# Optimization experiments

Hardware: AMD Instinct MI355X
Metric: run time of the kernel (lower is better)

## Reference

```python
import jax, jax.numpy as jnp
import numpy as np

D_MODEL = 768
NUM_HEADS = 12
D_K = D_MODEL // NUM_HEADS
B, S = 8, 1024


def setup_inputs() -> dict:
    key = jax.random.key(0)
    ks = jax.random.split(key, 10)
    sc = 1.0 / np.sqrt(D_MODEL)
    inp = {
        'x': jax.random.normal(ks[0], (B, S, D_MODEL), dtype=jnp.float32),
        'mask': jnp.tril(jnp.ones((1, 1, S, S), dtype=jnp.int32)),
        'W_q': jax.random.normal(ks[1], (D_MODEL, D_MODEL), jnp.float32) * sc,
        'b_q': jnp.zeros((D_MODEL,), jnp.float32),
        'W_k': jax.random.normal(ks[2], (D_MODEL, D_MODEL), jnp.float32) * sc,
        'b_k': jnp.zeros((D_MODEL,), jnp.float32),
        'W_v': jax.random.normal(ks[3], (D_MODEL, D_MODEL), jnp.float32) * sc,
        'b_v': jnp.zeros((D_MODEL,), jnp.float32),
        'W_o': jax.random.normal(ks[4], (D_MODEL, D_MODEL), jnp.float32) * sc,
        'b_o': jnp.zeros((D_MODEL,), jnp.float32),
    }
    return inp


def reference(x, mask, W_q, b_q, W_k, b_k, W_v, b_v, W_o, b_o):
    b, s, d = x.shape
    # project (torch Linear: y = x @ W.T + b; here weights stored as [in, out])
    q = (x @ W_q + b_q).reshape(b, s, NUM_HEADS, D_K).transpose(0, 2, 1, 3)
    k = (x @ W_k + b_k).reshape(b, s, NUM_HEADS, D_K).transpose(0, 2, 1, 3)
    v = (x @ W_v + b_v).reshape(b, s, NUM_HEADS, D_K).transpose(0, 2, 1, 3)
    scores = jnp.einsum('bhqd,bhkd->bhqk', q, k) / jnp.sqrt(jnp.float32(D_K))
    scores = jnp.where(mask == 0, jnp.float32(-jnp.inf), scores)
    attn = jax.nn.softmax(scores, axis=-1)  # dropout: eval mode (identity)
    out = jnp.einsum('bhqk,bhkd->bhqd', attn, v)
    out = out.transpose(0, 2, 1, 3).reshape(b, s, d)
    return out @ W_o + b_o
```

## Files before the change

### kernel.cpp

```cpp
#include <hip/hip_runtime.h>
#include <hip/hip_bf16.h>
#include <stdint.h>

typedef __attribute__((ext_vector_type(8))) short short8;
typedef __attribute__((ext_vector_type(4))) short s16x4;
typedef __attribute__((ext_vector_type(4))) float f32x4;

#define GLDS16(gp, lp) __builtin_amdgcn_global_load_lds( \
    (const __attribute__((address_space(1))) void*)(gp), \
    (__attribute__((address_space(3))) void*)(lp), 16, 0, 0)

__device__ __forceinline__ unsigned short f2bf(float f) {
  union { float f; unsigned u; } v; v.f = f;
  unsigned r = v.u + 0x7FFFu + ((v.u >> 16) & 1u);
  return (unsigned short)(r >> 16);
}

__device__ __forceinline__ short bfpack(float f) {
  union { float f; unsigned u; } v; v.f = f;
  return (short)((v.u + 0x8000u) >> 16);
}

__global__ __launch_bounds__(256) void cast_x(const float* __restrict__ x,
                                              unsigned short* __restrict__ o, int n4) {
  int i = blockIdx.x * 256 + threadIdx.x;
  if (i < n4) {
    float4 v = ((const float4*)x)[i];
    union { unsigned short u[4]; unsigned long long ll; } r;
    r.u[0] = f2bf(v.x); r.u[1] = f2bf(v.y); r.u[2] = f2bf(v.z); r.u[3] = f2bf(v.w);
    ((unsigned long long*)o)[i] = r.ll;
  }
}

__global__ __launch_bounds__(256) void cast_wt4(const float* __restrict__ W0,
                                                const float* __restrict__ W1,
                                                const float* __restrict__ W2,
                                                const float* __restrict__ W3,
                                                unsigned short* __restrict__ T0,
                                                unsigned short* __restrict__ T1,
                                                unsigned short* __restrict__ T2,
                                                unsigned short* __restrict__ T3) {
  __shared__ float t[16][17];
  const int z = blockIdx.z;
  const float* W = z == 0 ? W0 : (z == 1 ? W1 : (z == 2 ? W2 : W3));
  unsigned short* Wt = z == 0 ? T0 : (z == 1 ? T1 : (z == 2 ? T2 : T3));
  int tx = threadIdx.x, ty = threadIdx.y;
  int c0 = blockIdx.x * 16, r0 = blockIdx.y * 16;
  t[ty][tx] = W[(size_t)(r0 + ty) * 768 + c0 + tx];
  __syncthreads();
  Wt[(size_t)(c0 + ty) * 768 + r0 + tx] = f2bf(t[tx][ty]);
}

__device__ __forceinline__ void gemm_core(const unsigned short* __restrict__ A,
                                          const unsigned short* __restrict__ Bt,
                                          int row0, int col0, f32x4 acc[4][4],
                                          unsigned short* sA, unsigned short* sB) {
  const int t = threadIdx.x, l = t & 63;
  const int w = t >> 6, wr = w >> 1, wc = w & 1;
  const int lr = l & 15, lk = l >> 4;
  const int rs = t >> 2;
  const int csw = ((t & 3) ^ (rs & 3) ^ ((t >> 4) & 3)) * 8;
  const int rsw = (lr & 3) ^ (lr >> 2);
  const unsigned short* Ar = A + (size_t)(row0 + rs) * 768 + csw;
  const unsigned short* Br = Bt + (size_t)(col0 + rs) * 768 + csw;

#define GSTAGE(BUF, K0)                                                     \
  do {                                                                      \
    GLDS16(Ar + (K0), sA + (BUF) * 4096 + t * 8);                           \
    GLDS16(Ar + (size_t)64 * 768 + (K0), sA + (BUF) * 4096 + 2048 + t * 8); \
    GLDS16(Br + (K0), sB + (BUF) * 4096 + t * 8);                           \
    GLDS16(Br + (size_t)64 * 768 + (K0), sB + (BUF) * 4096 + 2048 + t * 8); \
  } while (0)

#define GCOMPUTE(BUF)                                                            \
  do {                                                                           \
    const unsigned short* cA = sA + (BUF) * 4096;                                \
    const unsigned short* cB = sB + (BUF) * 4096;                                \
    short8 af[4], bfr[4];                                                        \
    _Pragma("unroll") for (int i = 0; i < 4; ++i)                                \
        af[i] = *(const short8*)(cA + (wr * 64 + i * 16 + lr) * 32 + ((lk ^ rsw) * 8)); \
    _Pragma("unroll") for (int i = 0; i < 4; ++i)                                \
        bfr[i] = *(const short8*)(cB + (wc * 64 + i * 16 + lr) * 32 + ((lk ^ rsw) * 8)); \
    __builtin_amdgcn_s_setprio(1);                                               \
    _Pragma("unroll") for (int i = 0; i < 4; ++i)                                \
        _Pragma("unroll") for (int j = 0; j < 4; ++j)                            \
            acc[i][j] = __builtin_amdgcn_mfma_f32_16x16x32_bf16(af[i], bfr[j], acc[i][j], 0, 0, 0); \
    __builtin_amdgcn_s_setprio(0);                                               \
  } while (0)

  GSTAGE(0, 0);
  GSTAGE(1, 32);
  int b0 = 0, b2 = 2;
#pragma unroll 1
  for (int kt = 0; kt < 23; ++kt) {
    asm volatile("s_waitcnt vmcnt(4)" ::: "memory");
    __builtin_amdgcn_s_barrier();
    __builtin_amdgcn_sched_barrier(0);
    if (kt < 22) GSTAGE(b2, (kt + 2) * 32);
    GCOMPUTE(b0);
    b0 = (b0 == 2) ? 0 : b0 + 1;
    b2 = (b2 == 2) ? 0 : b2 + 1;
  }
  asm volatile("s_waitcnt vmcnt(0)" ::: "memory");
  __builtin_amdgcn_s_barrier();
  __builtin_amdgcn_sched_barrier(0);
  GCOMPUTE(b0);
#undef GSTAGE
#undef GCOMPUTE
}

__global__ __launch_bounds__(256, 3) void gemm_qkv(const unsigned short* __restrict__ A,
                                                   const unsigned short* __restrict__ Bt,
                                                   const float* __restrict__ bq,
                                                   const float* __restrict__ bk,
                                                   const float* __restrict__ bv,
                                                   unsigned short* __restrict__ Qb,
                                                   unsigned short* __restrict__ Kb,
                                                   unsigned short* __restrict__ Vt) {
  __shared__ unsigned short sA[3][4096];
  __shared__ unsigned short sB[3][4096];
  const int flat = blockIdx.x;
  const int xcd = flat & 7, idx = flat >> 3;
  const int brow = xcd * 8 + (idx & 7);
  const int bcol = idx >> 3;
  const int row0 = brow * 128, col0 = bcol * 128;
  f32x4 acc[4][4] = {};
  gemm_core(A, Bt, row0, col0, acc, &sA[0][0], &sB[0][0]);

  const int l = threadIdx.x & 63, w = threadIdx.x >> 6;
  const int wr = w >> 1, wc = w & 1, lr = l & 15, lk = l >> 4;
  const int which = bcol / 6;
  const int ncb = col0 - which * 768;
  if (which == 2) {
    const int bb = row0 >> 10;
    const int sb = (row0 & 1023) + wr * 64;
#pragma unroll
    for (int i = 0; i < 4; ++i) {
      const int sp = sb + (i >> 1) * 32 + lk * 8 + (i & 1) * 4;
#pragma unroll
      for (int j = 0; j < 4; ++j) {
        const int n = ncb + wc * 64 + j * 16 + lr;
        const float bn = bv[n];
        s16x4 vv;
#pragma unroll
        for (int r = 0; r < 4; ++r) vv[r] = (short)f2bf(acc[i][j][r] + bn);
        *(s16x4*)(Vt + ((size_t)(bb * 768 + n)) * 1024 + sp) = vv;
      }
    }
  } else {
    unsigned short* outp = which == 0 ? Qb : Kb;
    const float* bias = which == 0 ? bq : bk;
    const float scale = which == 0 ? 0.18033688011112042f : 1.0f;
#pragma unroll
    for (int i = 0; i < 4; ++i)
#pragma unroll
      for (int j = 0; j < 4; ++j) {
        int n = ncb + wc * 64 + j * 16 + lr;
        float bn = bias[n];
#pragma unroll
        for (int r = 0; r < 4; ++r) {
          int m = row0 + wr * 64 + i * 16 + lk * 4 + r;
          outp[(size_t)m * 768 + n] = f2bf((acc[i][j][r] + bn) * scale);
        }
      }
  }
}

__global__ __launch_bounds__(256, 3) void gemm_out(const unsigned short* __restrict__ A,
                                                   const unsigned short* __restrict__ Bt,
                                                   const float* __restrict__ bias,
                                                   float* __restrict__ C) {
  __shared__ unsigned short sA[3][4096];
  __shared__ unsigned short sB[3][4096];
  const int flat = blockIdx.x;
  const int xcd = flat & 7, idx = flat >> 3;
  const int brow = xcd * 8 + (idx & 7);
  const int bcol = idx >> 3;
  const int row0 = brow * 128, col0 = bcol * 128;
  f32x4 acc[4][4] = {};
  gemm_core(A, Bt, row0, col0, acc, &sA[0][0], &sB[0][0]);

  const int l = threadIdx.x & 63, w = threadIdx.x >> 6;
  const int wr = w >> 1, wc = w & 1, lr = l & 15, lk = l >> 4;
#pragma unroll
  for (int i = 0; i < 4; ++i)
#pragma unroll
    for (int j = 0; j < 4; ++j) {
      int n = col0 + wc * 64 + j * 16 + lr;
      float bn = bias[n];
#pragma unroll
      for (int r = 0; r < 4; ++r) {
        int m = row0 + wr * 64 + i * 16 + lk * 4 + r;
        C[(size_t)m * 768 + n] = acc[i][j][r] + bn;
      }
    }
}

__global__ __launch_bounds__(256, 3) void attn(const unsigned short* __restrict__ Q,
                                               const unsigned short* __restrict__ Kg,
                                               const unsigned short* __restrict__ V2,
                                               unsigned short* __restrict__ O) {
  __shared__ unsigned short Kl[3][4096];
  __shared__ unsigned short Vl[3][4096];
  const int tid = threadIdx.x;
  const int l = tid & 63, w = tid >> 6;
  const int lr = l & 15, lk = l >> 4;
  const int o = blockIdx.x;
  const int b = o & 7, rem = o >> 3, pair = rem & 7, h = rem >> 3;
  const int hd = h * 64;
  const size_t bS = (size_t)b * 1024;
  const unsigned short* Kbase = Kg + bS * 768 + hd;
  const unsigned short* Vbase = V2 + ((size_t)b * 768 + hd) * 1024;
  const int rs = tid >> 3;
  const int kcol = ((tid & 7) ^ (rs & 7)) * 8;
  const int swz = (lr & 7);
  const int qloc = w * 16 + lr;

#define STAGE(BUF, T)                                                          \
  do {                                                                         \
    const size_t kv0_ = (size_t)(T) * 64;                                      \
    GLDS16(Kbase + (kv0_ + rs) * 768 + kcol, &Kl[BUF][tid * 8]);               \
    GLDS16(Kbase + (kv0_ + rs + 32) * 768 + kcol, &Kl[BUF][(256 + tid) * 8]);  \
    GLDS16(Vbase + (size_t)rs * 1024 + kv0_ + kcol, &Vl[BUF][tid * 8]);        \
    GLDS16(Vbase + (size_t)(rs + 32) * 1024 + kv0_ + kcol,                     \
           &Vl[BUF][(256 + tid) * 8]);                                         \
  } while (0)

#pragma unroll 1
  for (int half = 0; half < 2; ++half) {
    const int qt = half ? 15 - pair : pair;
    const int qw = qt * 64 + w * 16;
    const int ntile = qt + 1;
    __syncthreads();
    short8 bq0, bq1;
    {
      size_t qb = (bS + qw + lr) * 768 + hd + lk * 8;
      bq0 = *(const short8*)(Q + qb);
      bq1 = *(const short8*)(Q + qb + 32);
    }
    f32x4 oc0 = {}, oc1 = {}, oc2 = {}, oc3 = {};
    float lsum = 0.f;

    STAGE(0, 0);
    if (ntile > 1) STAGE(1, 1);
    int b0 = 0, b2 = 2;

#pragma unroll 1
    for (int t = 0; t < ntile; ++t) {
      if (t < ntile - 1) {
        asm volatile("s_waitcnt vmcnt(4)" ::: "memory");
      } else {
        asm volatile("s_waitcnt vmcnt(0)" ::: "memory");
      }
      __builtin_amdgcn_s_barrier();
      __builtin_amdgcn_sched_barrier(0);
      if (t + 2 < ntile) STAGE(b2, t + 2);
      const unsigned short* Kb_ = Kl[b0];
      const unsigned short* Vb_ = Vl[b0];
      b0 = (b0 == 2) ? 0 : b0 + 1;
      b2 = (b2 == 2) ? 0 : b2 + 1;
      short8 kf00 = *(const short8*)(Kb_ + (0 * 16 + lr) * 64 + (((0 * 4 + lk) ^ swz) * 8));
      short8 kf01 = *(const short8*)(Kb_ + (0 * 16 + lr) * 64 + (((1 * 4 + lk) ^ swz) * 8));
      short8 kf10 = *(const short8*)(Kb_ + (1 * 16 + lr) * 64 + (((0 * 4 + lk) ^ swz) * 8));
      short8 kf11 = *(const short8*)(Kb_ + (1 * 16 + lr) * 64 + (((1 * 4 + lk) ^ swz) * 8));
      short8 kf20 = *(const short8*)(Kb_ + (2 * 16 + lr) * 64 + (((0 * 4 + lk) ^ swz) * 8));
      short8 kf21 = *(const short8*)(Kb_ + (2 * 16 + lr) * 64 + (((1 * 4 + lk) ^ swz) * 8));
      short8 kf30 = *(const short8*)(Kb_ + (3 * 16 + lr) * 64 + (((0 * 4 + lk) ^ swz) * 8));
      short8 kf31 = *(const short8*)(Kb_ + (3 * 16 + lr) * 64 + (((1 * 4 + lk) ^ swz) * 8));
      short8 vf00 = *(const short8*)(Vb_ + (0 * 16 + lr) * 64 + (((0 * 4 + lk) ^ swz) * 8));
      short8 vf01 = *(const short8*)(Vb_ + (0 * 16 + lr) * 64 + (((1 * 4 + lk) ^ swz) * 8));
      short8 vf10 = *(const short8*)(Vb_ + (1 * 16 + lr) * 64 + (((0 * 4 + lk) ^ swz) * 8));
      short8 vf11 = *(const short8*)(Vb_ + (1 * 16 + lr) * 64 + (((1 * 4 + lk) ^ swz) * 8));
      short8 vf20 = *(const short8*)(Vb_ + (2 * 16 + lr) * 64 + (((0 * 4 + lk) ^ swz) * 8));
      short8 vf21 = *(const short8*)(Vb_ + (2 * 16 + lr) * 64 + (((1 * 4 + lk) ^ swz) * 8));
      short8 vf30 = *(const short8*)(Vb_ + (3 * 16 + lr) * 64 + (((0 * 4 + lk) ^ swz) * 8));
      short8 vf31 = *(const short8*)(Vb_ + (3 * 16 + lr) * 64 + (((1 * 4 + lk) ^ swz) * 8));

      f32x4 s0 = {}, s1 = {}, s2 = {}, s3 = {};
      __builtin_amdgcn_s_setprio(1);
      s0 = __builtin_amdgcn_mfma_f32_16x16x32_bf16(kf00, bq0, s0, 0, 0, 0);
      s0 = __builtin_amdgcn_mfma_f32_16x16x32_bf16(kf01, bq1, s0, 0, 0, 0);
      s1 = __builtin_amdgcn_mfma_f32_16x16x32_bf16(kf10, bq0, s1, 0, 0, 0);
      s1 = __builtin_amdgcn_mfma_f32_16x16x32_bf16(kf11, bq1, s1, 0, 0, 0);
      s2 = __builtin_amdgcn_mfma_f32_16x16x32_bf16(kf20, bq0, s2, 0, 0, 0);
      s2 = __builtin_amdgcn_mfma_f32_16x16x32_bf16(kf21, bq1, s2, 0, 0, 0);
      s3 = __builtin_amdgcn_mfma_f32_16x16x32_bf16(kf30, bq0, s3, 0, 0, 0);
      s3 = __builtin_amdgcn_mfma_f32_16x16x32_bf16(kf31, bq1, s3, 0, 0, 0);
      __builtin_amdgcn_s_setprio(0);

      if (t == ntile - 1) {
        const int kb = lk * 4;
#pragma unroll
        for (int r = 0; r < 4; ++r) {
          if (kb + 0 + r > qloc) s0[r] = -1e30f;
          if (kb + 16 + r > qloc) s1[r] = -1e30f;
          if (kb + 32 + r > qloc) s2[r] = -1e30f;
          if (kb + 48 + r > qloc) s3[r] = -1e30f;
        }
      }
      float p0[4], p1[4], p2[4], p3[4];
#pragma unroll
      for (int r = 0; r < 4; ++r) {
        p0[r] = __builtin_amdgcn_exp2f(s0[r]);
        p1[r] = __builtin_amdgcn_exp2f(s1[r]);
        p2[r] = __builtin_amdgcn_exp2f(s2[r]);
        p3[r] = __builtin_amdgcn_exp2f(s3[r]);
      }
      lsum += ((p0[0] + p0[1]) + (p0[2] + p0[3])) + ((p1[0] + p1[1]) + (p1[2] + p1[3])) +
              ((p2[0] + p2[1]) + (p2[2] + p2[3])) + ((p3[0] + p3[1]) + (p3[2] + p3[3]));
      short8 pb0, pb1;
#pragma unroll
      for (int r = 0; r < 4; ++r) {
        pb0[r] = bfpack(p0[r]); pb0[r + 4] = bfpack(p1[r]);
        pb1[r] = bfpack(p2[r]); pb1[r + 4] = bfpack(p3[r]);
      }
      __builtin_amdgcn_s_setprio(1);
      oc0 = __builtin_amdgcn_mfma_f32_16x16x32_bf16(vf00, pb0, oc0, 0, 0, 0);
      oc0 = __builtin_amdgcn_mfma_f32_16x16x32_bf16(vf01, pb1, oc0, 0, 0, 0);
      oc1 = __builtin_amdgcn_mfma_f32_16x16x32_bf16(vf10, pb0, oc1, 0, 0, 0);
      oc1 = __builtin_amdgcn_mfma_f32_16x16x32_bf16(vf11, pb1, oc1, 0, 0, 0);
      oc2 = __builtin_amdgcn_mfma_f32_16x16x32_bf16(vf20, pb0, oc2, 0, 0, 0);
      oc2 = __builtin_amdgcn_mfma_f32_16x16x32_bf16(vf21, pb1, oc2, 0, 0, 0);
      oc3 = __builtin_amdgcn_mfma_f32_16x16x32_bf16(vf30, pb0, oc3, 0, 0, 0);
      oc3 = __builtin_amdgcn_mfma_f32_16x16x32_bf16(vf31, pb1, oc3, 0, 0, 0);
      __builtin_amdgcn_s_setprio(0);
    }

    lsum += __shfl_xor(lsum, 16);
    lsum += __shfl_xor(lsum, 32);
    const float inv = 1.f / lsum;
    unsigned short* op = O + (bS + qw + lr) * 768 + hd + lk * 4;
    s16x4 o0, o1, o2, o3;
#pragma unroll
    for (int r = 0; r < 4; ++r) {
      o0[r] = (short)f2bf(oc0[r] * inv);
      o1[r] = (short)f2bf(oc1[r] * inv);
      o2[r] = (short)f2bf(oc2[r] * inv);
      o3[r] = (short)f2bf(oc3[r] * inv);
    }
    *(s16x4*)(op) = o0;
    *(s16x4*)(op + 16) = o1;
    *(s16x4*)(op + 32) = o2;
    *(s16x4*)(op + 48) = o3;
  }
#undef STAGE
}

extern "C" void kernel_launch(void* const* d_in, const int* in_sizes, int n_in,
                              void* d_out, int out_size, void* d_ws, size_t ws_size,
                              hipStream_t stream) {
  const float* x  = (const float*)d_in[0];
  const float* Wq = (const float*)d_in[2]; const float* bq = (const float*)d_in[3];
  const float* Wk = (const float*)d_in[4]; const float* bk = (const float*)d_in[5];
  const float* Wv = (const float*)d_in[6]; const float* bv = (const float*)d_in[7];
  const float* Wo = (const float*)d_in[8]; const float* bo = (const float*)d_in[9];
  float* out = (float*)d_out;

  char* ws = (char*)d_ws;
  unsigned short* xb  = (unsigned short*)ws;
  unsigned short* WtQ = (unsigned short*)(ws + (size_t)12582912);
  unsigned short* WtK = WtQ + 589824;
  unsigned short* WtV = WtK + 589824;
  unsigned short* WtO = WtV + 589824;
  unsigned short* Qb  = (unsigned short*)(ws + (size_t)12582912 + (size_t)4 * 1179648);
  unsigned short* Kb  = Qb + 6291456;
  unsigned short* Vt  = Kb + 2 * 6291456;
  unsigned short* Ob  = xb;

  cast_x<<<6144, 256, 0, stream>>>(x, xb, 1572864);
  cast_wt4<<<dim3(48, 48, 4), dim3(16, 16), 0, stream>>>(Wq, Wk, Wv, Wo, WtQ, WtK, WtV, WtO);
  gemm_qkv<<<1152, 256, 0, stream>>>(xb, WtQ, bq, bk, bv, Qb, Kb, Vt);
  attn<<<768, 256, 0, stream>>>(Qb, Kb, Vt, Ob);
  gemm_out<<<384, 256, 0, stream>>>(Ob, WtO, bo, out);
}
```

Baseline: 105.6 us.

## Replace QKV GEMM with 256x256-tile, 8-wave double-buffered kernel

The fused QKV projection moves from 128x128 tiles with 4 waves and a triple-buffered 32-wide K pipeline to 256x256 tiles with 8 waves. The new kernel uses a double-buffered 64-wide K step, split into halves with interleaved LDS reads, async global-to-LDS loads and MFMA phases under raised priority. Larger tiles raise arithmetic intensity and cut global/L2 traffic per flop, and the grid is remapped for XCD locality. In exchange, 288 blocks is close to the CU count of the device, so wave quantization and lower occupancy are risks, as are higher register use and more barriers per step.

```diff
diff --git a/kernel.cpp b/kernel.cpp
--- a/kernel.cpp
+++ b/kernel.cpp
@@ -51,6 +51,170 @@
   Wt[(size_t)(c0 + ty) * 768 + r0 + tx] = f2bf(t[tx][ty]);
 }
 
+__global__ __launch_bounds__(512, 2) void gemm_qkv8(const unsigned short* __restrict__ A,
+                                                    const unsigned short* __restrict__ Bt,
+                                                    const float* __restrict__ bq,
+                                                    const float* __restrict__ bk,
+                                                    const float* __restrict__ bv,
+                                                    unsigned short* __restrict__ Qb,
+                                                    unsigned short* __restrict__ Kb,
+                                                    unsigned short* __restrict__ Vt) {
+  __shared__ unsigned short lA[2][2][8192];
+  __shared__ unsigned short lB[2][2][8192];
+  const int tid = threadIdx.x;
+  const int l = tid & 63;
+  const int wid = tid >> 6, wr = wid >> 2, wc = wid & 3;
+  const int lr = l & 15, lk = l >> 4;
+  const int rsw = (lr & 3) ^ (lr >> 2);
+  const int bid = blockIdx.x;
+  const int wgid = (bid & 7) * 36 + (bid >> 3);
+  const int brow = wgid & 31, bcol = wgid >> 5;
+  const int row0 = brow * 256, col0 = bcol * 256;
+  const int r0s = tid >> 2;
+  const int r1s = (512 + tid) >> 2;
+  const int c0s = ((tid & 3) ^ (r0s & 3) ^ ((r0s >> 2) & 3)) * 8;
+  const int c1s = ((tid & 3) ^ (r1s & 3) ^ ((r1s >> 2) & 3)) * 8;
+  const unsigned short* Ar0 = A + (size_t)(row0 + r0s) * 768 + c0s;
+  const unsigned short* Ar1 = A + (size_t)(row0 + r1s) * 768 + c1s;
+  const unsigned short* Br0 = Bt + (size_t)(col0 + r0s) * 768 + c0s;
+  const unsigned short* Br1 = Bt + (size_t)(col0 + r1s) * 768 + c1s;
+
+#define STA8(DB, H, KT)                                               \
+  do {                                                                \
+    const int k0_ = (KT) * 64 + (H) * 32;                             \
+    GLDS16(Ar0 + k0_, &lA[DB][H][tid * 8]);                           \
+    GLDS16(Ar1 + k0_, &lA[DB][H][(512 + tid) * 8]);                   \
+  } while (0)
+#define STB8(DB, H, KT)                                               \
+  do {                                                                \
+    const int k0_ = (KT) * 64 + (H) * 32;                             \
+    GLDS16(Br0 + k0_, &lB[DB][H][tid * 8]);                           \
+    GLDS16(Br1 + k0_, &lB[DB][H][(512 + tid) * 8]);                   \
+  } while (0)
+#define RDA8(DB, S, I) (*(const short8*)(&lA[DB][S][(wr * 128 + (I) * 16 + lr) * 32 + (lk ^ rsw) * 8]))
+#define RDB8(DB, S, J) (*(const short8*)(&lB[DB][S][(wc * 64 + (J) * 16 + lr) * 32 + (lk ^ rsw) * 8]))
+
+  f32x4 acc[8][4] = {};
+  STA8(0, 0, 0); STB8(0, 0, 0); STA8(0, 1, 0); STB8(0, 1, 0);
+
+#pragma unroll 1
+  for (int kt = 0; kt < 12; ++kt) {
+    const int cur = kt & 1, nxt = cur ^ 1;
+    short8 af[4], bf[4];
+    asm volatile("s_waitcnt vmcnt(4)" ::: "memory");
+    __builtin_amdgcn_s_barrier();
+    __builtin_amdgcn_sched_barrier(0);
+#pragma unroll
+    for (int i = 0; i < 4; ++i) af[i] = RDA8(cur, 0, i);
+#pragma unroll
+    for (int j = 0; j < 4; ++j) bf[j] = RDB8(cur, 0, j);
+    if (kt < 11) STA8(nxt, 0, kt + 1);
+    asm volatile("s_waitcnt lgkmcnt(0)" ::: "memory");
+    __builtin_amdgcn_sched_barrier(0);
+    __builtin_amdgcn_s_setprio(1);
+#pragma unroll
+    for (int i = 0; i < 4; ++i)
+#pragma unroll
+      for (int j = 0; j < 4; ++j)
+        acc[i][j] = __builtin_amdgcn_mfma_f32_16x16x32_bf16(af[i], bf[j], acc[i][j], 0, 0, 0);
+    __builtin_amdgcn_s_setprio(0);
+    __builtin_amdgcn_s_barrier();
+    __builtin_amdgcn_sched_barrier(0);
+#pragma unroll
+    for (int i = 0; i < 4; ++i) af[i] = RDA8(cur, 0, 4 + i);
+    if (kt < 11) STB8(nxt, 0, kt + 1);
+    asm volatile("s_waitcnt lgkmcnt(0)" ::: "memory");
+    __builtin_amdgcn_sched_barrier(0);
+    __builtin_amdgcn_s_setprio(1);
+#pragma unroll
+    for (int i = 0; i < 4; ++i)
+#pragma unroll
+      for (int j = 0; j < 4; ++j)
+        acc[4 + i][j] = __builtin_amdgcn_mfma_f32_16x16x32_bf16(af[i], bf[j], acc[4 + i][j], 0, 0, 0);
+    __builtin_amdgcn_s_setprio(0);
+    __builtin_amdgcn_s_barrier();
+    __builtin_amdgcn_sched_barrier(0);
+    if (kt < 11) {
+      asm volatile("s_waitcnt vmcnt(4)" ::: "memory");
+    } else {
+      asm volatile("s_waitcnt vmcnt(0)" ::: "memory");
+    }
+    __builtin_amdgcn_s_barrier();
+    __builtin_amdgcn_sched_barrier(0);
+#pragma unroll
+    for (int i = 0; i < 4; ++i) af[i] = RDA8(cur, 1, i);
+#pragma unroll
+    for (int j = 0; j < 4; ++j) bf[j] = RDB8(cur, 1, j);
+    if (kt < 11) STA8(nxt, 1, kt + 1);
+    asm volatile("s_waitcnt lgkmcnt(0)" ::: "memory");
+    __builtin_amdgcn_sched_barrier(0);
+    __builtin_amdgcn_s_setprio(1);
+#pragma unroll
+    for (int i = 0; i < 4; ++i)
+#pragma unroll
+      for (int j = 0; j < 4; ++j)
+        acc[i][j] = __builtin_amdgcn_mfma_f32_16x16x32_bf16(af[i], bf[j], acc[i][j], 0, 0, 0);
+    __builtin_amdgcn_s_setprio(0);
+    __builtin_amdgcn_s_barrier();
+    __builtin_amdgcn_sched_barrier(0);
+#pragma unroll
+    for (int i = 0; i < 4; ++i) af[i] = RDA8(cur, 1, 4 + i);
+    if (kt < 11) STB8(nxt, 1, kt + 1);
+    asm volatile("s_waitcnt lgkmcnt(0)" ::: "memory");
+    __builtin_amdgcn_sched_barrier(0);
+    __builtin_amdgcn_s_setprio(1);
+#pragma unroll
+    for (int i = 0; i < 4; ++i)
+#pragma unroll
+      for (int j = 0; j < 4; ++j)
+        acc[4 + i][j] = __builtin_amdgcn_mfma_f32_16x16x32_bf16(af[i], bf[j], acc[4 + i][j], 0, 0, 0);
+    __builtin_amdgcn_s_setprio(0);
+    __builtin_amdgcn_s_barrier();
+    __builtin_amdgcn_sched_barrier(0);
+  }
+#undef STA8
+#undef STB8
+#undef RDA8
+#undef RDB8
+
+  const int which = bcol / 3;
+  const int ncb = col0 - which * 768;
+  if (which == 2) {
+    const int mb = row0 + wr * 128;
+    const int bb = mb >> 10;
+    const int sbase = mb & 1023;
+#pragma unroll
+    for (int i = 0; i < 8; ++i) {
+      const int sp = sbase + (i >> 1) * 32 + lk * 8 + (i & 1) * 4;
+#pragma unroll
+      for (int j = 0; j < 4; ++j) {
+        const int n = ncb + wc * 64 + j * 16 + lr;
+        const float bn = bv[n];
+        s16x4 vv;
+#pragma unroll
+        for (int r = 0; r < 4; ++r) vv[r] = (short)f2bf(acc[i][j][r] + bn);
+        *(s16x4*)(Vt + ((size_t)(bb * 768 + n)) * 1024 + sp) = vv;
+      }
+    }
+  } else {
+    unsigned short* outp = which == 0 ? Qb : Kb;
+    const float* bias = which == 0 ? bq : bk;
+    const float scale = which == 0 ? 0.18033688011112042f : 1.0f;
+#pragma unroll
+    for (int i = 0; i < 8; ++i)
+#pragma unroll
+      for (int j = 0; j < 4; ++j) {
+        const int n = ncb + wc * 64 + j * 16 + lr;
+        const float bn = bias[n];
+#pragma unroll
+        for (int r = 0; r < 4; ++r) {
+          const int m = row0 + wr * 128 + i * 16 + lk * 4 + r;
+          outp[(size_t)m * 768 + n] = f2bf((acc[i][j][r] + bn) * scale);
+        }
+      }
+  }
+}
+
 __device__ __forceinline__ void gemm_core(const unsigned short* __restrict__ A,
                                           const unsigned short* __restrict__ Bt,
                                           int row0, int col0, f32x4 acc[4][4],
@@ -107,63 +271,6 @@
   GCOMPUTE(b0);
 #undef GSTAGE
 #undef GCOMPUTE
-}
-
-__global__ __launch_bounds__(256, 3) void gemm_qkv(const unsigned short* __restrict__ A,
-                                                   const unsigned short* __restrict__ Bt,
-                                                   const float* __restrict__ bq,
-                                                   const float* __restrict__ bk,
-                                                   const float* __restrict__ bv,
-                                                   unsigned short* __restrict__ Qb,
-                                                   unsigned short* __restrict__ Kb,
-                                                   unsigned short* __restrict__ Vt) {
-  __shared__ unsigned short sA[3][4096];
-  __shared__ unsigned short sB[3][4096];
-  const int flat = blockIdx.x;
-  const int xcd = flat & 7, idx = flat >> 3;
-  const int brow = xcd * 8 + (idx & 7);
-  const int bcol = idx >> 3;
-  const int row0 = brow * 128, col0 = bcol * 128;
-  f32x4 acc[4][4] = {};
-  gemm_core(A, Bt, row0, col0, acc, &sA[0][0], &sB[0][0]);
-
-  const int l = threadIdx.x & 63, w = threadIdx.x >> 6;
-  const int wr = w >> 1, wc = w & 1, lr = l & 15, lk = l >> 4;
-  const int which = bcol / 6;
-  const int ncb = col0 - which * 768;
-  if (which == 2) {
-    const int bb = row0 >> 10;
-    const int sb = (row0 & 1023) + wr * 64;
-#pragma unroll
-    for (int i = 0; i < 4; ++i) {
-      const int sp = sb + (i >> 1) * 32 + lk * 8 + (i & 1) * 4;
-#pragma unroll
-      for (int j = 0; j < 4; ++j) {
-        const int n = ncb + wc * 64 + j * 16 + lr;
-        const float bn = bv[n];
-        s16x4 vv;
-#pragma unroll
-        for (int r = 0; r < 4; ++r) vv[r] = (short)f2bf(acc[i][j][r] + bn);
-        *(s16x4*)(Vt + ((size_t)(bb * 768 + n)) * 1024 + sp) = vv;
-      }
-    }
-  } else {
-    unsigned short* outp = which == 0 ? Qb : Kb;
-    const float* bias = which == 0 ? bq : bk;
-    const float scale = which == 0 ? 0.18033688011112042f : 1.0f;
-#pragma unroll
-    for (int i = 0; i < 4; ++i)
-#pragma unroll
-      for (int j = 0; j < 4; ++j) {
-        int n = ncb + wc * 64 + j * 16 + lr;
-        float bn = bias[n];
-#pragma unroll
-        for (int r = 0; r < 4; ++r) {
-          int m = row0 + wr * 64 + i * 16 + lk * 4 + r;
-          outp[(size_t)m * 768 + n] = f2bf((acc[i][j][r] + bn) * scale);
-        }
-      }
-  }
 }
 
 __global__ __launch_bounds__(256, 3) void gemm_out(const unsigned short* __restrict__ A,
@@ -369,7 +476,7 @@
 
   cast_x<<<6144, 256, 0, stream>>>(x, xb, 1572864);
   cast_wt4<<<dim3(48, 48, 4), dim3(16, 16), 0, stream>>>(Wq, Wk, Wv, Wo, WtQ, WtK, WtV, WtO);
-  gemm_qkv<<<1152, 256, 0, stream>>>(xb, WtQ, bq, bk, bv, Qb, Kb, Vt);
+  gemm_qkv8<<<288, 512, 0, stream>>>(xb, WtQ, bq, bk, bv, Qb, Kb, Vt);
   attn<<<768, 256, 0, stream>>>(Qb, Kb, Vt, Ob);
   gemm_out<<<384, 256, 0, stream>>>(Ob, WtO, bo, out);
 }
```

Measured after the change: 120.5 us. 1.14x slower.
